# Optimization experiments

Measured on AMD Instinct MI355X. Metric: run time of the kernel, lower is better.

## Reference

```python
import jax, jax.numpy as jnp
import numpy as np

B, L, D, H = 8, 1024, 1024, 16
DH = D // H  # dim_per_head = 64
HG = H // 2  # global/local head split


def setup_inputs() -> dict:
    key = jax.random.key(0)
    ks = jax.random.split(key, 10)
    s = 1.0 / np.sqrt(D)
    return {
        "key": jax.random.normal(ks[0], (B, L, D), jnp.float32),
        "value": jax.random.normal(ks[1], (B, L, D), jnp.float32),
        "query": jax.random.normal(ks[2], (B, L, D), jnp.float32),
        "mask": jax.random.bernoulli(ks[3], 0.1, (B, L, L)),
        "additional_mask": jax.random.bernoulli(ks[4], 0.1, (B, L)),
        "Wk": jax.random.normal(ks[5], (D, D), jnp.float32) * s,
        "bk": jnp.zeros((D,), jnp.float32),
        "Wv": jax.random.normal(ks[6], (D, D), jnp.float32) * s,
        "bv": jnp.zeros((D,), jnp.float32),
        "Wq": jax.random.normal(ks[7], (D, D), jnp.float32) * s,
        "bq": jnp.zeros((D,), jnp.float32),
        "Wo": jax.random.normal(ks[8], (D, D), jnp.float32) * s,
        "bo": jnp.zeros((D,), jnp.float32),
    }


def _shape(x):
    # [B, L, D] -> [B, H, L, DH]
    return x.reshape(B, -1, H, DH).transpose(0, 2, 1, 3)


def reference(key, value, query, mask, additional_mask,
              Wk, bk, Wv, bv, Wq, bq, Wo, bo):
    # projections (torch Linear: x @ W.T + b)
    k = _shape(key @ Wk.T + bk)
    v = _shape(value @ Wv.T + bv)
    q = _shape(query @ Wq.T + bq) * (1.0 / np.sqrt(DH))  # scale query (edge_feature=None, additional_mask given)

    qg, ql = q[:, :HG], q[:, HG:]
    kg, kl = k[:, :HG], k[:, HG:]
    vg, vl = v[:, :HG], v[:, HG:]

    # global heads: standard masked attention
    score_g = jnp.einsum('bhqd,bhkd->bhqk', qg, kg)
    top_score = score_g[:, 0]  # taken BEFORE masking, as in original
    score_g = jnp.where(mask[:, None, :, :], -1e18, score_g)
    attn_g = jax.nn.softmax(score_g, axis=-1)  # dropout = identity (eval)
    ctx_g = jnp.einsum('bhqk,bhkd->bhqd', attn_g, vg)

    # local heads: additional_mask [B, k] broadcast over heads and queries
    score_l = jnp.einsum('bhqd,bhkd->bhqk', ql, kl)
    score_l = jnp.where(additional_mask[:, None, None, :], -1e18, score_l)
    attn_l = jax.nn.softmax(score_l, axis=-1)
    ctx_l = jnp.einsum('bhqk,bhkd->bhqd', attn_l, vl)

    ctx = jnp.concatenate([ctx_g, ctx_l], axis=1)          # [B, H, L, DH]
    ctx = ctx.transpose(0, 2, 1, 3).reshape(B, -1, D)      # unshape -> [B, L, D]
    out = ctx @ Wo.T + bo
    return out, top_score
```

## Files before the change

kernel.cpp:

```cpp
#include <hip/hip_runtime.h>
#include <hip/hip_bf16.h>

typedef unsigned short u16;
typedef unsigned int u32;
typedef __attribute__((ext_vector_type(8))) short short8;
typedef __attribute__((ext_vector_type(4))) short short4v;
typedef __attribute__((ext_vector_type(4))) float floatx4;

#define BB 8
#define LL 1024
#define DD 1024
#define HH 16
#define DHH 64
#define NEGBIG (-3.0e38f)
#define QSCALE 0.1803368801111204f
#define LN2F   0.6931471805599453f

__device__ inline u16 f2b(float f) {
  union { __hip_bfloat16 h; u16 u; } cv;
  cv.h = __float2bfloat16(f);
  return cv.u;
}
__device__ inline float b2f(u16 u) {
  union { u16 u; __hip_bfloat16 h; } cv;
  cv.u = u;
  return __bfloat162float(cv.h);
}
__device__ inline float fin(float v, float sentinel) {
  return (fabsf(v) < 1e30f) ? v : sentinel;
}
__device__ inline float fexp2(float x) {
#if __has_builtin(__builtin_amdgcn_exp2f)
  return __builtin_amdgcn_exp2f(x);
#else
  return exp2f(x);
#endif
}
__device__ inline void async16(const void* g, void* l) {
  __builtin_amdgcn_global_load_lds(
      (__attribute__((address_space(1))) void*)(const_cast<void*>(g)),
      (__attribute__((address_space(3))) void*)l, 16, 0, 0);
}


__global__ __launch_bounds__(256) void convpack(
    const float* __restrict__ key, const float* __restrict__ value,
    const float* __restrict__ Wk, const float* __restrict__ Wv,
    const float* __restrict__ Wq, const float* __restrict__ Wo,
    const int* __restrict__ mask, const int* __restrict__ amask,
    u16* __restrict__ keyb, u16* __restrict__ valb, u16* __restrict__ Wkb,
    u16* __restrict__ Wvb, u16* __restrict__ Wqb, u16* __restrict__ Wob,
    u32* __restrict__ maskb, u32* __restrict__ amaskb) {
  const int job = blockIdx.y;
  const int gtid = blockIdx.x * 256 + threadIdx.x;
  const int stride = gridDim.x * 256;

  if (job < 6) {
    const float* src; u16* dst; size_t n4;
    switch (job) {
      case 0: src = key;   dst = keyb; n4 = (size_t)BB * LL * DD / 4; break;
      case 1: src = value; dst = valb; n4 = (size_t)BB * LL * DD / 4; break;
      case 2: src = Wk;    dst = Wkb;  n4 = (size_t)DD * DD / 4; break;
      case 3: src = Wv;    dst = Wvb;  n4 = (size_t)DD * DD / 4; break;
      case 4: src = Wq;    dst = Wqb;  n4 = (size_t)DD * DD / 4; break;
      default: src = Wo;   dst = Wob;  n4 = (size_t)DD * DD / 4; break;
    }
    for (size_t i = gtid; i < n4; i += stride) {
      float4 v = ((const float4*)src)[i];
      short4v s;
      s[0] = (short)f2b(v.x); s[1] = (short)f2b(v.y);
      s[2] = (short)f2b(v.z); s[3] = (short)f2b(v.w);
      *(short4v*)(dst + i * 4) = s;
    }
  } else if (job == 6) {
    const size_t nw = (size_t)BB * LL * LL / 32;
    for (size_t w = gtid; w < nw; w += stride) {
      const int4* src = (const int4*)(mask + w * 32);
      u32 bits = 0;
#pragma unroll
      for (int c = 0; c < 8; c++) {
        int4 v = src[c];
        bits |= (u32)(v.x != 0) << (c * 4);
        bits |= (u32)(v.y != 0) << (c * 4 + 1);
        bits |= (u32)(v.z != 0) << (c * 4 + 2);
        bits |= (u32)(v.w != 0) << (c * 4 + 3);
      }
      maskb[w] = bits;
    }
  } else {
    const int nw = BB * LL / 32;
    for (int w = gtid; w < nw; w += stride) {
      const int4* src = (const int4*)(amask + w * 32);
      u32 bits = 0;
#pragma unroll
      for (int c = 0; c < 8; c++) {
        int4 v = src[c];
        bits |= (u32)(v.x != 0) << (c * 4);
        bits |= (u32)(v.y != 0) << (c * 4 + 1);
        bits |= (u32)(v.z != 0) << (c * 4 + 2);
        bits |= (u32)(v.w != 0) << (c * 4 + 3);
      }
      amaskb[w] = bits;
    }
  }
}

__global__ __launch_bounds__(256) void gemm_qkv(
    const u16* __restrict__ keyb, const u16* __restrict__ valb,
    const float* __restrict__ query, const u16* __restrict__ Wkb,
    const u16* __restrict__ Wvb, const u16* __restrict__ Wqb,
    const float* __restrict__ bk, const float* __restrict__ bv,
    const float* __restrict__ bq, u16* __restrict__ kbuf,
    u16* __restrict__ vbt, u16* __restrict__ qbuf) {
  __shared__ u16 As[128 * 32];
  __shared__ u16 Ws[128 * 32];

  const int z = blockIdx.z;
  const int tid = threadIdx.x;
  const int wave = tid >> 6, lane = tid & 63;
  const int lr = lane & 15, lq = lane >> 4;
  const int row0 = blockIdx.x * 128;
  const int col0 = blockIdx.y * 128;
  const int wm = (wave & 1) * 64, wn = (wave >> 1) * 64;

  floatx4 acc[4][4];
#pragma unroll
  for (int i = 0; i < 4; i++)
#pragma unroll
    for (int j = 0; j < 4; j++) acc[i][j] = (floatx4){0.f, 0.f, 0.f, 0.f};

  const int cc0 = tid, cc1 = 256 + tid;
  u16* As0 = As + wave * 512;
  u16* As1 = As + 2048 + wave * 512;
  u16* Ws0 = Ws + wave * 512;
  u16* Ws1 = Ws + 2048 + wave * 512;

  if (z < 2) {
    const u16* A  = (z == 0) ? keyb : valb;
    const u16* Wb = (z == 0) ? Wkb : Wvb;
    const u16* Ag0 = A + (size_t)(row0 + (cc0 >> 2)) * 1024 + (cc0 & 3) * 8;
    const u16* Ag1 = A + (size_t)(row0 + (cc1 >> 2)) * 1024 + (cc1 & 3) * 8;
    const u16* Wg0 = Wb + (size_t)(col0 + (cc0 >> 2)) * 1024 + (cc0 & 3) * 8;
    const u16* Wg1 = Wb + (size_t)(col0 + (cc1 >> 2)) * 1024 + (cc1 & 3) * 8;

    for (int k0 = 0; k0 < 1024; k0 += 32) {
      __syncthreads();
      async16(Ag0 + k0, As0);
      async16(Ag1 + k0, As1);
      async16(Wg0 + k0, Ws0);
      async16(Wg1 + k0, Ws1);
      __syncthreads();

      short8 af[4], wf[4];
#pragma unroll
      for (int mi = 0; mi < 4; mi++)
        af[mi] = *(const short8*)(As + (wm + mi * 16 + lr) * 32 + lq * 8);
#pragma unroll
      for (int ni = 0; ni < 4; ni++)
        wf[ni] = *(const short8*)(Ws + (wn + ni * 16 + lr) * 32 + lq * 8);
#pragma unroll
      for (int mi = 0; mi < 4; mi++)
#pragma unroll
        for (int ni = 0; ni < 4; ni++)
          acc[mi][ni] = __builtin_amdgcn_mfma_f32_16x16x32_bf16(af[mi], wf[ni],
                                                                acc[mi][ni], 0, 0, 0);
    }
  } else {
    const u16* Wg0 = Wqb + (size_t)(col0 + (cc0 >> 2)) * 1024 + (cc0 & 3) * 8;
    const u16* Wg1 = Wqb + (size_t)(col0 + (cc1 >> 2)) * 1024 + (cc1 & 3) * 8;

    for (int k0 = 0; k0 < 1024; k0 += 32) {
      float4 ag[4];
#pragma unroll
      for (int it = 0; it < 4; it++) {
        const int cc = it * 256 + tid;
        ag[it] = *(const float4*)(query + (size_t)(row0 + (cc >> 3)) * 1024 +
                                  (cc & 7) * 4 + k0);
      }
      __syncthreads();
      async16(Wg0 + k0, Ws0);
      async16(Wg1 + k0, Ws1);
#pragma unroll
      for (int it = 0; it < 4; it++) {
        const int cc = it * 256 + tid;
        short4v s;
        s[0] = (short)f2b(ag[it].x); s[1] = (short)f2b(ag[it].y);
        s[2] = (short)f2b(ag[it].z); s[3] = (short)f2b(ag[it].w);
        *(short4v*)(As + (cc >> 3) * 32 + (cc & 7) * 4) = s;
      }
      __syncthreads();

      short8 af[4], wf[4];
#pragma unroll
      for (int mi = 0; mi < 4; mi++)
        af[mi] = *(const short8*)(As + (wm + mi * 16 + lr) * 32 + lq * 8);
#pragma unroll
      for (int ni = 0; ni < 4; ni++)
        wf[ni] = *(const short8*)(Ws + (wn + ni * 16 + lr) * 32 + lq * 8);
#pragma unroll
      for (int mi = 0; mi < 4; mi++)
#pragma unroll
        for (int ni = 0; ni < 4; ni++)
          acc[mi][ni] = __builtin_amdgcn_mfma_f32_16x16x32_bf16(af[mi], wf[ni],
                                                                acc[mi][ni], 0, 0, 0);
    }
  }

  const float scale = (z == 2) ? QSCALE : 1.0f;
  const float* bias = (z == 0) ? bk : (z == 1) ? bv : bq;
  u16* outb = (z == 0) ? kbuf : qbuf;

#pragma unroll
  for (int ni = 0; ni < 4; ni++) {
    const int col = col0 + wn + ni * 16 + lr;
    const float bvv = bias[col];
#pragma unroll
    for (int mi = 0; mi < 4; mi++) {
#pragma unroll
      for (int r = 0; r < 4; r++) {
        const int row = row0 + wm + mi * 16 + lq * 4 + r;
        const float v = (acc[mi][ni][r] + bvv) * scale;
        const int b = row >> 10, l = row & 1023, h = col >> 6, dh = col & 63;
        if (z == 1)
          vbt[((b * HH + h) * DHH + dh) * LL + l] = f2b(v);
        else
          outb[((b * HH + h) * LL + l) * DHH + dh] = f2b(v);
      }
    }
  }
}

template <int OUT>
__global__ __launch_bounds__(256) void gemm_b(
    const u16* __restrict__ A, const u16* __restrict__ Wb,
    const float* __restrict__ bias, void* __restrict__ outv, float scale) {
  __shared__ u16 As[128 * 32];
  __shared__ u16 Ws[128 * 32];

  const int tid = threadIdx.x;
  const int wave = tid >> 6, lane = tid & 63;
  const int lr = lane & 15, lq = lane >> 4;
  const int row0 = blockIdx.x * 128;
  const int col0 = blockIdx.y * 128;
  const int wm = (wave & 1) * 64, wn = (wave >> 1) * 64;

  floatx4 acc[4][4];
#pragma unroll
  for (int i = 0; i < 4; i++)
#pragma unroll
    for (int j = 0; j < 4; j++) acc[i][j] = (floatx4){0.f, 0.f, 0.f, 0.f};

  const int cc0 = tid, cc1 = 256 + tid;
  const u16* Ag0 = A + (size_t)(row0 + (cc0 >> 2)) * 1024 + (cc0 & 3) * 8;
  const u16* Ag1 = A + (size_t)(row0 + (cc1 >> 2)) * 1024 + (cc1 & 3) * 8;
  const u16* Wg0 = Wb + (size_t)(col0 + (cc0 >> 2)) * 1024 + (cc0 & 3) * 8;
  const u16* Wg1 = Wb + (size_t)(col0 + (cc1 >> 2)) * 1024 + (cc1 & 3) * 8;
  u16* As0 = As + wave * 512;
  u16* As1 = As + 2048 + wave * 512;
  u16* Ws0 = Ws + wave * 512;
  u16* Ws1 = Ws + 2048 + wave * 512;

  for (int k0 = 0; k0 < 1024; k0 += 32) {
    __syncthreads();
    async16(Ag0 + k0, As0);
    async16(Ag1 + k0, As1);
    async16(Wg0 + k0, Ws0);
    async16(Wg1 + k0, Ws1);
    __syncthreads();

    short8 af[4], wf[4];
#pragma unroll
    for (int mi = 0; mi < 4; mi++)
      af[mi] = *(const short8*)(As + (wm + mi * 16 + lr) * 32 + lq * 8);
#pragma unroll
    for (int ni = 0; ni < 4; ni++)
      wf[ni] = *(const short8*)(Ws + (wn + ni * 16 + lr) * 32 + lq * 8);
#pragma unroll
    for (int mi = 0; mi < 4; mi++)
#pragma unroll
      for (int ni = 0; ni < 4; ni++)
        acc[mi][ni] = __builtin_amdgcn_mfma_f32_16x16x32_bf16(af[mi], wf[ni],
                                                              acc[mi][ni], 0, 0, 0);
  }

#pragma unroll
  for (int ni = 0; ni < 4; ni++) {
    const int col = col0 + wn + ni * 16 + lr;
    const float bv = bias[col];
#pragma unroll
    for (int mi = 0; mi < 4; mi++) {
#pragma unroll
      for (int r = 0; r < 4; r++) {
        const int row = row0 + wm + mi * 16 + lq * 4 + r;
        const float v = (acc[mi][ni][r] + bv) * scale;
        if (OUT == 0) {
          const int b = row >> 10, l = row & 1023, h = col >> 6, dh = col & 63;
          ((u16*)outv)[((b * HH + h) * LL + l) * DHH + dh] = f2b(v);
        } else if (OUT == 2) {
          const int b = row >> 10, l = row & 1023, h = col >> 6, dh = col & 63;
          ((u16*)outv)[((b * HH + h) * DHH + dh) * LL + l] = f2b(v);
        } else {
          ((float*)outv)[(size_t)row * 1024 + col] = v;
        }
      }
    }
  }
}

__global__ __launch_bounds__(256) void attn_fast(
    const u16* __restrict__ qbuf, const u16* __restrict__ kbuf,
    const u16* __restrict__ vbt, const u32* __restrict__ maskb,
    const u32* __restrict__ amaskb, u16* __restrict__ ctx,
    float* __restrict__ top) {
  __shared__ u16 Ks[2][64 * 64];
  __shared__ u16 Vts[2][64 * 64];

  const int id = blockIdx.x;
  const int xcd = id & 7;
  const int r_ = id >> 3;
  const int b = r_ & 7;
  const int h = (((r_ >> 3) & 1) << 3) | (xcd ^ b);
  const int qt = r_ >> 4;

  const int tid = threadIdx.x, wave = tid >> 6, lane = tid & 63;
  const int lr = lane & 15, lq = lane >> 4;
  const int lq4 = lq * 4;
  const int x7 = lr & 7;

  const u16* Qg = qbuf + (size_t)((b * HH + h) * LL + qt * 128) * DHH;
  const u16* Kg = kbuf + (size_t)((b * HH + h) * LL) * DHH;
  const u16* Vtg = vbt + (size_t)((b * HH + h) * DHH) * LL;

  short8 qf[2][2];
#pragma unroll
  for (int mi = 0; mi < 2; mi++)
#pragma unroll
    for (int kk = 0; kk < 2; kk++)
      qf[mi][kk] = *(const short8*)(Qg + (wave * 32 + mi * 16 + lr) * 64 +
                                    kk * 32 + lq * 8);

  const int g0 = tid, g1 = 256 + tid;
  const int kr0 = g0 >> 3, kc0 = (g0 & 7) ^ (kr0 & 7);
  const int kr1 = g1 >> 3, kc1 = (g1 & 7) ^ (kr1 & 7);
  const int cs0 = ((0 + lq) ^ x7) * 8;
  const int cs1 = ((4 + lq) ^ x7) * 8;
  const int lqh = lq >> 1, lqb = (lq & 1) * 4;
  const int go00 = ((0 + lqh) ^ x7) * 8 + lqb;
  const int go01 = ((2 + lqh) ^ x7) * 8 + lqb;
  const int go10 = ((4 + lqh) ^ x7) * 8 + lqb;
  const int go11 = ((6 + lqh) ^ x7) * 8 + lqb;

  auto stage = [&](int kc, int buf) {
    async16(Kg + kc * 4096 + kr0 * 64 + kc0 * 8, &Ks[buf][wave * 512]);
    async16(Kg + kc * 4096 + kr1 * 64 + kc1 * 8, &Ks[buf][2048 + wave * 512]);
    async16(Vtg + (size_t)kr0 * LL + kc * 64 + kc0 * 8, &Vts[buf][wave * 512]);
    async16(Vtg + (size_t)kr1 * LL + kc * 64 + kc1 * 8,
            &Vts[buf][2048 + wave * 512]);
  };

  float mrow[2], lrow[2];
  floatx4 Oacc[2][4];
#pragma unroll
  for (int mi = 0; mi < 2; mi++) {
    mrow[mi] = NEGBIG;
    lrow[mi] = 0.f;
#pragma unroll
    for (int ni = 0; ni < 4; ni++) Oacc[mi][ni] = (floatx4){0.f, 0.f, 0.f, 0.f};
  }

  stage(0, 0);

  for (int kc = 0; kc < 16; kc++) {
    const int cur = kc & 1;
    __syncthreads();
    if (kc < 15) stage(kc + 1, cur ^ 1);
    const u16* Ksc = Ks[cur];
    const u16* Vtsc = Vts[cur];

    floatx4 S[2][4];
    __builtin_amdgcn_s_setprio(1);
#pragma unroll
    for (int nj = 0; nj < 4; nj++) {
      const short8 kf0 = *(const short8*)(Ksc + (nj * 16 + lr) * 64 + cs0);
      const short8 kf1 = *(const short8*)(Ksc + (nj * 16 + lr) * 64 + cs1);
#pragma unroll
      for (int mi = 0; mi < 2; mi++) {
        floatx4 z = (floatx4){0.f, 0.f, 0.f, 0.f};
        z = __builtin_amdgcn_mfma_f32_16x16x32_bf16(kf1, qf[mi][1], z, 0, 0, 0);
        z = __builtin_amdgcn_mfma_f32_16x16x32_bf16(kf0, qf[mi][0], z, 0, 0, 0);
        S[mi][nj] = z;
      }
    }
    __builtin_amdgcn_s_setprio(0);

    short8 pf[2][2];
#pragma unroll
    for (int mi = 0; mi < 2; mi++) {
      const int row = qt * 128 + wave * 32 + mi * 16 + lr;

      if (h == 0) {
        float* tp = top + (size_t)(b * LL + row) * LL + kc * 64 + lq4;
#pragma unroll
        for (int nj = 0; nj < 4; nj++) {
          float4 t;
          t.x = S[mi][nj][0] * LN2F; t.y = S[mi][nj][1] * LN2F;
          t.z = S[mi][nj][2] * LN2F; t.w = S[mi][nj][3] * LN2F;
          *(float4*)(tp + nj * 16) = t;
        }
      }

      if (h < 8) {
        const uint2 mw =
            *(const uint2*)(maskb + (size_t)(b * LL + row) * 32 + kc * 2);
#pragma unroll
        for (int nj = 0; nj < 4; nj++) {
          const u32 nib = (((nj & 2) ? mw.y : mw.x) >> ((nj & 1) * 16 + lq4)) & 15u;
#pragma unroll
          for (int r = 0; r < 4; r++)
            if ((nib >> r) & 1) S[mi][nj][r] = -1e18f;
        }
      } else {
        const uint2 aw = *(const uint2*)(amaskb + b * 32 + kc * 2);
#pragma unroll
        for (int nj = 0; nj < 4; nj++) {
          const u32 nib = (((nj & 2) ? aw.y : aw.x) >> ((nj & 1) * 16 + lq4)) & 15u;
#pragma unroll
          for (int r = 0; r < 4; r++)
            if ((nib >> r) & 1) S[mi][nj][r] = -1e18f;
        }
      }

      float cm = fmaxf(fmaxf(S[mi][0][0], S[mi][0][1]),
                       fmaxf(S[mi][0][2], S[mi][0][3]));
#pragma unroll
      for (int nj = 1; nj < 4; nj++)
        cm = fmaxf(cm, fmaxf(fmaxf(S[mi][nj][0], S[mi][nj][1]),
                             fmaxf(S[mi][nj][2], S[mi][nj][3])));
      cm = fmaxf(cm, __shfl_xor(cm, 16, 64));
      cm = fmaxf(cm, __shfl_xor(cm, 32, 64));
      const float mold = mrow[mi];
      const float mnew = fmaxf(mold, cm);
      const float alpha = fexp2(mold - mnew);
      mrow[mi] = mnew;
      float rs = 0.f;
#pragma unroll
      for (int nj = 0; nj < 4; nj++)
#pragma unroll
        for (int r = 0; r < 4; r++) {
          const float p = fexp2(S[mi][nj][r] - mnew);
          S[mi][nj][r] = p;
          rs += p;
        }
      rs += __shfl_xor(rs, 16, 64);
      rs += __shfl_xor(rs, 32, 64);
      lrow[mi] = lrow[mi] * alpha + rs;
#pragma unroll
      for (int ni = 0; ni < 4; ni++)
#pragma unroll
        for (int r = 0; r < 4; r++) Oacc[mi][ni][r] *= alpha;

#pragma unroll
      for (int kk = 0; kk < 2; kk++) {
        short8 p;
#pragma unroll
        for (int r = 0; r < 4; r++) {
          p[r] = (short)f2b(S[mi][2 * kk][r]);
          p[4 + r] = (short)f2b(S[mi][2 * kk + 1][r]);
        }
        pf[mi][kk] = p;
      }
    }

    __builtin_amdgcn_s_setprio(1);
#pragma unroll
    for (int ni = 0; ni < 4; ni++) {
      const int rb = (ni * 16 + lr) * 64;
      const short4v v00 = *(const short4v*)(Vtsc + rb + go00);
      const short4v v01 = *(const short4v*)(Vtsc + rb + go01);
      const short4v v10 = *(const short4v*)(Vtsc + rb + go10);
      const short4v v11 = *(const short4v*)(Vtsc + rb + go11);
      const short8 vf0 = __builtin_shufflevector(v00, v01, 0, 1, 2, 3, 4, 5, 6, 7);
      const short8 vf1 = __builtin_shufflevector(v10, v11, 0, 1, 2, 3, 4, 5, 6, 7);
#pragma unroll
      for (int mi = 0; mi < 2; mi++) {
        Oacc[mi][ni] =
            __builtin_amdgcn_mfma_f32_16x16x32_bf16(vf0, pf[mi][0], Oacc[mi][ni], 0, 0, 0);
        Oacc[mi][ni] =
            __builtin_amdgcn_mfma_f32_16x16x32_bf16(vf1, pf[mi][1], Oacc[mi][ni], 0, 0, 0);
      }
    }
    __builtin_amdgcn_s_setprio(0);
  }

#pragma unroll
  for (int mi = 0; mi < 2; mi++) {
    const float inv = 1.0f / lrow[mi];
    const int row = qt * 128 + wave * 32 + mi * 16 + lr;
    u16* cp = ctx + (size_t)(b * LL + row) * DD + h * DHH + lq4;
#pragma unroll
    for (int ni = 0; ni < 4; ni++) {
      short4v o;
      o[0] = (short)f2b(Oacc[mi][ni][0] * inv);
      o[1] = (short)f2b(Oacc[mi][ni][1] * inv);
      o[2] = (short)f2b(Oacc[mi][ni][2] * inv);
      o[3] = (short)f2b(Oacc[mi][ni][3] * inv);
      *(short4v*)(cp + ni * 16) = o;
    }
  }
}

template <int MODE>
__global__ __launch_bounds__(256) void gemm_k(
    const void* __restrict__ Av, const float* __restrict__ W,
    const float* __restrict__ biasp, void* __restrict__ outv, float scale) {
  __shared__ u16 As[128 * 32];
  __shared__ u16 Ws[128 * 32];
  const int tid = threadIdx.x;
  const int wave = tid >> 6, lane = tid & 63;
  const int lr = lane & 15, lq = lane >> 4;
  const int row0 = blockIdx.x * 128;
  const int col0 = blockIdx.y * 128;
  const int wm = (wave & 1) * 64, wn = (wave >> 1) * 64;
  floatx4 acc[4][4];
#pragma unroll
  for (int i = 0; i < 4; i++)
#pragma unroll
    for (int j = 0; j < 4; j++) acc[i][j] = (floatx4){0.f, 0.f, 0.f, 0.f};
  const float* Af = (const float*)Av;
  const u16* Ab = (const u16*)Av;
  for (int k0 = 0; k0 < 1024; k0 += 32) {
    float4 wg[4];
#pragma unroll
    for (int it = 0; it < 4; it++) {
      const int cc = it * 256 + tid;
      wg[it] = *(const float4*)(W + (size_t)(col0 + (cc >> 3)) * 1024 + (cc & 7) * 4 + k0);
    }
    float4 ag[4];
    short8 ab0, ab1;
    if (MODE == 0) {
#pragma unroll
      for (int it = 0; it < 4; it++) {
        const int cc = it * 256 + tid;
        ag[it] = *(const float4*)(Af + (size_t)(row0 + (cc >> 3)) * 1024 + (cc & 7) * 4 + k0);
      }
    } else {
      const int cc0 = tid, cc1 = 256 + tid;
      ab0 = *(const short8*)(Ab + (size_t)(row0 + (cc0 >> 2)) * 1024 + (cc0 & 3) * 8 + k0);
      ab1 = *(const short8*)(Ab + (size_t)(row0 + (cc1 >> 2)) * 1024 + (cc1 & 3) * 8 + k0);
    }
    __syncthreads();
#pragma unroll
    for (int it = 0; it < 4; it++) {
      const int cc = it * 256 + tid;
      short4v s;
      s[0] = (short)f2b(wg[it].x); s[1] = (short)f2b(wg[it].y);
      s[2] = (short)f2b(wg[it].z); s[3] = (short)f2b(wg[it].w);
      *(short4v*)(Ws + (cc >> 3) * 32 + (cc & 7) * 4) = s;
    }
    if (MODE == 0) {
#pragma unroll
      for (int it = 0; it < 4; it++) {
        const int cc = it * 256 + tid;
        short4v s;
        s[0] = (short)f2b(ag[it].x); s[1] = (short)f2b(ag[it].y);
        s[2] = (short)f2b(ag[it].z); s[3] = (short)f2b(ag[it].w);
        *(short4v*)(As + (cc >> 3) * 32 + (cc & 7) * 4) = s;
      }
    } else {
      *(short8*)(As + tid * 8) = ab0;
      *(short8*)(As + (256 + tid) * 8) = ab1;
    }
    __syncthreads();
    short8 af[4], wf[4];
#pragma unroll
    for (int mi = 0; mi < 4; mi++)
      af[mi] = *(const short8*)(As + (wm + mi * 16 + lr) * 32 + lq * 8);
#pragma unroll
    for (int ni = 0; ni < 4; ni++)
      wf[ni] = *(const short8*)(Ws + (wn + ni * 16 + lr) * 32 + lq * 8);
#pragma unroll
    for (int mi = 0; mi < 4; mi++)
#pragma unroll
      for (int ni = 0; ni < 4; ni++)
        acc[mi][ni] = __builtin_amdgcn_mfma_f32_16x16x32_bf16(af[mi], wf[ni], acc[mi][ni], 0, 0, 0);
  }
#pragma unroll
  for (int ni = 0; ni < 4; ni++) {
    const int col = col0 + wn + ni * 16 + lr;
    const float bv = biasp[col];
#pragma unroll
    for (int mi = 0; mi < 4; mi++) {
#pragma unroll
      for (int r = 0; r < 4; r++) {
        const int row = row0 + wm + mi * 16 + lq * 4 + r;
        float v = (acc[mi][ni][r] + bv) * scale;
        v = fin(v, MODE == 0 ? 700.0f : 1000.0f);
        if (MODE == 0) {
          const int b = row >> 10, l = row & 1023, h = col >> 6, dh = col & 63;
          ((u16*)outv)[((b * HH + h) * LL + l) * DHH + dh] = f2b(v);
        } else {
          ((float*)outv)[(size_t)row * 1024 + col] = v;
        }
      }
    }
  }
}

__global__ __launch_bounds__(256) void attn_kernel(
    const u16* __restrict__ qbuf, const u16* __restrict__ kbuf,
    const u16* __restrict__ vbuf, const int* __restrict__ mask,
    const int* __restrict__ amask, u16* __restrict__ ctx,
    float* __restrict__ top) {
  __shared__ u16 Qs[128 * 64];
  __shared__ u16 Ks[64 * 64];
  __shared__ u16 Vts[64 * 64];
  __shared__ u16 Ps[4][32 * 64];
  const int qt = blockIdx.x, h = blockIdx.y, b = blockIdx.z;
  const int tid = threadIdx.x, wave = tid >> 6, lane = tid & 63;
  const int lr = lane & 15, lq = lane >> 4;
  const u16* Qg = qbuf + (size_t)((b * HH + h) * LL + qt * 128) * DHH;
  const u16* Kg = kbuf + (size_t)((b * HH + h) * LL) * DHH;
  const u16* Vg = vbuf + (size_t)((b * HH + h) * LL) * DHH;
#pragma unroll
  for (int it = 0; it < 4; it++) {
    short8 qv = *(const short8*)(Qg + (it * 256 + tid) * 8);
    *(short8*)(Qs + (it * 256 + tid) * 8) = qv;
  }
  float mrow[2][4], lrow[2][4];
  floatx4 Oacc[2][4];
#pragma unroll
  for (int mi = 0; mi < 2; mi++)
#pragma unroll
    for (int r = 0; r < 4; r++) { mrow[mi][r] = NEGBIG; lrow[mi][r] = 0.f; }
#pragma unroll
  for (int mi = 0; mi < 2; mi++)
#pragma unroll
    for (int ni = 0; ni < 4; ni++) Oacc[mi][ni] = (floatx4){0.f, 0.f, 0.f, 0.f};
  for (int kc = 0; kc < 16; kc++) {
    const u16* Kc = Kg + kc * 64 * DHH;
    const u16* Vc = Vg + kc * 64 * DHH;
    short8 kv0 = *(const short8*)(Kc + tid * 8);
    short8 kv1 = *(const short8*)(Kc + (256 + tid) * 8);
    short8 vv0 = *(const short8*)(Vc + tid * 8);
    short8 vv1 = *(const short8*)(Vc + (256 + tid) * 8);
    __syncthreads();
    *(short8*)(Ks + tid * 8) = kv0;
    *(short8*)(Ks + (256 + tid) * 8) = kv1;
    {
      const int r0 = tid >> 3, e0 = (tid & 7) * 8;
#pragma unroll
      for (int j = 0; j < 8; j++) Vts[(e0 + j) * 64 + r0] = (u16)vv0[j];
      const int cc1 = 256 + tid;
      const int r1 = cc1 >> 3, e1 = (cc1 & 7) * 8;
#pragma unroll
      for (int j = 0; j < 8; j++) Vts[(e1 + j) * 64 + r1] = (u16)vv1[j];
    }
    __syncthreads();
    floatx4 S[2][4];
    short8 qf[2][2];
#pragma unroll
    for (int mi = 0; mi < 2; mi++)
#pragma unroll
      for (int kk = 0; kk < 2; kk++)
        qf[mi][kk] = *(const short8*)(Qs + (wave * 32 + mi * 16 + lr) * 64 + kk * 32 + lq * 8);
#pragma unroll
    for (int nj = 0; nj < 4; nj++) {
      short8 kf0 = *(const short8*)(Ks + (nj * 16 + lr) * 64 + lq * 8);
      short8 kf1 = *(const short8*)(Ks + (nj * 16 + lr) * 64 + 32 + lq * 8);
#pragma unroll
      for (int mi = 0; mi < 2; mi++) {
        floatx4 z = (floatx4){0.f, 0.f, 0.f, 0.f};
        z = __builtin_amdgcn_mfma_f32_16x16x32_bf16(qf[mi][1], kf1, z, 0, 0, 0);
        z = __builtin_amdgcn_mfma_f32_16x16x32_bf16(qf[mi][0], kf0, z, 0, 0, 0);
        S[mi][nj] = z;
      }
    }
#pragma unroll
    for (int mi = 0; mi < 2; mi++)
#pragma unroll
      for (int nj = 0; nj < 4; nj++)
#pragma unroll
        for (int r = 0; r < 4; r++) S[mi][nj][r] = fin(S[mi][nj][r], 800.0f);
    if (h == 0) {
#pragma unroll
      for (int mi = 0; mi < 2; mi++)
#pragma unroll
        for (int nj = 0; nj < 4; nj++)
#pragma unroll
          for (int r = 0; r < 4; r++) {
            const int row = qt * 128 + wave * 32 + mi * 16 + lq * 4 + r;
            const int colk = kc * 64 + nj * 16 + lr;
            top[(size_t)(b * LL + row) * LL + colk] = S[mi][nj][r];
          }
    }
    if (h < 8) {
#pragma unroll
      for (int mi = 0; mi < 2; mi++)
#pragma unroll
        for (int r = 0; r < 4; r++) {
          const int row = qt * 128 + wave * 32 + mi * 16 + lq * 4 + r;
          const int* mp = mask + (size_t)(b * LL + row) * LL + kc * 64;
#pragma unroll
          for (int nj = 0; nj < 4; nj++) {
            const int mv = mp[nj * 16 + lr];
            S[mi][nj][r] = mv ? -1e18f : S[mi][nj][r];
          }
        }
    } else {
#pragma unroll
      for (int nj = 0; nj < 4; nj++) {
        const int mv = amask[b * LL + kc * 64 + nj * 16 + lr];
        if (mv) {
#pragma unroll
          for (int mi = 0; mi < 2; mi++)
#pragma unroll
            for (int r = 0; r < 4; r++) S[mi][nj][r] = -1e18f;
        }
      }
    }
#pragma unroll
    for (int mi = 0; mi < 2; mi++) {
#pragma unroll
      for (int r = 0; r < 4; r++) {
        float cm = S[mi][0][r];
#pragma unroll
        for (int nj = 1; nj < 4; nj++) cm = fmaxf(cm, S[mi][nj][r]);
#pragma unroll
        for (int off = 1; off < 16; off <<= 1) cm = fmaxf(cm, __shfl_xor(cm, off, 64));
        const float mold = mrow[mi][r];
        const float mnew = fmaxf(mold, cm);
        const float alpha = __expf(mold - mnew);
        mrow[mi][r] = mnew;
        float rs = 0.f;
#pragma unroll
        for (int nj = 0; nj < 4; nj++) {
          const float p = __expf(S[mi][nj][r] - mnew);
          S[mi][nj][r] = p;
          rs += p;
        }
#pragma unroll
        for (int off = 1; off < 16; off <<= 1) rs += __shfl_xor(rs, off, 64);
        lrow[mi][r] = lrow[mi][r] * alpha + rs;
#pragma unroll
        for (int ni = 0; ni < 4; ni++) Oacc[mi][ni][r] *= alpha;
      }
    }
#pragma unroll
    for (int mi = 0; mi < 2; mi++)
#pragma unroll
      for (int nj = 0; nj < 4; nj++)
#pragma unroll
        for (int r = 0; r < 4; r++)
          Ps[wave][(mi * 16 + lq * 4 + r) * 64 + nj * 16 + lr] = f2b(S[mi][nj][r]);
    __syncthreads();
#pragma unroll
    for (int kk = 0; kk < 2; kk++) {
      short8 pf[2];
#pragma unroll
      for (int mi = 0; mi < 2; mi++)
        pf[mi] = *(const short8*)(&Ps[wave][(mi * 16 + lr) * 64 + kk * 32 + lq * 8]);
#pragma unroll
      for (int ni = 0; ni < 4; ni++) {
        short8 vf = *(const short8*)(Vts + (ni * 16 + lr) * 64 + kk * 32 + lq * 8);
#pragma unroll
        for (int mi = 0; mi < 2; mi++)
          Oacc[mi][ni] = __builtin_amdgcn_mfma_f32_16x16x32_bf16(pf[mi], vf, Oacc[mi][ni], 0, 0, 0);
      }
    }
  }
#pragma unroll
  for (int mi = 0; mi < 2; mi++)
#pragma unroll
    for (int r = 0; r < 4; r++) {
      const float inv = 1.0f / lrow[mi][r];
      const int row = qt * 128 + wave * 32 + mi * 16 + lq * 4 + r;
#pragma unroll
      for (int ni = 0; ni < 4; ni++) {
        const int col = h * DHH + ni * 16 + lr;
        ctx[(size_t)(b * LL + row) * DD + col] = f2b(fin(Oacc[mi][ni][r] * inv, 900.0f));
      }
    }
}

extern "C" void kernel_launch(void* const* d_in, const int* in_sizes, int n_in,
                              void* d_out, int out_size, void* d_ws, size_t ws_size,
                              hipStream_t stream) {
  const float* key   = (const float*)d_in[0];
  const float* value = (const float*)d_in[1];
  const float* query = (const float*)d_in[2];
  const int* mask    = (const int*)d_in[3];
  const int* amask   = (const int*)d_in[4];
  const float* Wk = (const float*)d_in[5];
  const float* bk = (const float*)d_in[6];
  const float* Wv = (const float*)d_in[7];
  const float* bv = (const float*)d_in[8];
  const float* Wq = (const float*)d_in[9];
  const float* bq = (const float*)d_in[10];
  const float* Wo = (const float*)d_in[11];
  const float* bo = (const float*)d_in[12];

  float* outp = (float*)d_out;
  float* topp = outp + (size_t)BB * LL * DD;

  const size_t M8 = (size_t)BB * LL * DD;
  const size_t M1 = (size_t)DD * DD;
  const size_t NEED = (size_t)90 * 1024 * 1024;

  dim3 tb(256), gg(64, 8, 1), ga(8, 16, 8);

  if (ws_size >= NEED) {
    u16* W16 = (u16*)d_ws;
    u16* keyb = W16;
    u16* valb = W16 + M8;
    u16* qbuf = W16 + 2 * M8;
    u16* Wkb = W16 + 3 * M8;
    u16* Wvb = Wkb + M1;
    u16* Wqb = Wvb + M1;
    u16* Wob = Wqb + M1;
    u32* maskb = (u32*)(Wob + M1);
    u32* amaskb = maskb + 262144;
    u16* kbuf = W16 + 3 * M8 + 5 * M1;
    u16* vbt  = kbuf + M8;
    u16* cbuf = valb;

    convpack<<<dim3(256, 8), tb, 0, stream>>>(
        key, value, Wk, Wv, Wq, Wo, mask, amask,
        keyb, valb, Wkb, Wvb, Wqb, Wob, maskb, amaskb);
    gemm_qkv<<<dim3(64, 8, 3), tb, 0, stream>>>(
        keyb, valb, query, Wkb, Wvb, Wqb, bk, bv, bq, kbuf, vbt, qbuf);
    attn_fast<<<dim3(1024, 1, 1), tb, 0, stream>>>(qbuf, kbuf, vbt, maskb,
                                                   amaskb, cbuf, topp);
    gemm_b<1><<<gg, tb, 0, stream>>>(cbuf, Wob, bo, outp, 1.0f);
  } else {
    u16* kbuf = (u16*)d_ws;
    u16* vbuf = kbuf + M8;
    u16* qbuf = vbuf + M8;
    u16* cbuf = qbuf + M8;
    gemm_k<0><<<gg, tb, 0, stream>>>(key,   Wk, bk, kbuf, 1.0f);
    gemm_k<0><<<gg, tb, 0, stream>>>(value, Wv, bv, vbuf, 1.0f);
    gemm_k<0><<<gg, tb, 0, stream>>>(query, Wq, bq, qbuf, 0.125f);
    attn_kernel<<<ga, tb, 0, stream>>>(qbuf, kbuf, vbuf, mask, amask, cbuf, topp);
    gemm_k<1><<<gg, tb, 0, stream>>>(cbuf, Wo, bo, outp, 1.0f);
  }
}
```

Before: 428.4 us.

## Fuse key/value bf16 conversion into QKV GEMM, double-buffer it, defer softmax rescale

The separate fp32-to-bf16 conversion of key and value is removed from convpack. gemm_qkv now loads fp32 activations for all three projections and converts them in registers, which avoids writing and re-reading two large bf16 intermediates. The GEMM main loop is double-buffered in LDS, so the next tile's W async load and A register load overlap the MFMAs, with one barrier per iteration. In attention, mask words are prefetched one chunk ahead and the global/local mask branches are unified. The online-softmax rescale is skipped unless the running max grows by more than a threshold, which trades exactness of the running max for fewer exp and multiply operations and relies on exp2 headroom to avoid overflow.

```diff
diff --git a/kernel.cpp b/kernel.cpp
--- a/kernel.cpp
+++ b/kernel.cpp
@@ -15,6 +15,7 @@
 #define NEGBIG (-3.0e38f)
 #define QSCALE 0.1803368801111204f
 #define LN2F   0.6931471805599453f
+#define DEFER_THR 12.0f
 
 __device__ inline u16 f2b(float f) {
   union { __hip_bfloat16 h; u16 u; } cv;
@@ -44,27 +45,24 @@
 
 
 __global__ __launch_bounds__(256) void convpack(
-    const float* __restrict__ key, const float* __restrict__ value,
     const float* __restrict__ Wk, const float* __restrict__ Wv,
     const float* __restrict__ Wq, const float* __restrict__ Wo,
     const int* __restrict__ mask, const int* __restrict__ amask,
-    u16* __restrict__ keyb, u16* __restrict__ valb, u16* __restrict__ Wkb,
-    u16* __restrict__ Wvb, u16* __restrict__ Wqb, u16* __restrict__ Wob,
-    u32* __restrict__ maskb, u32* __restrict__ amaskb) {
+    u16* __restrict__ Wkb, u16* __restrict__ Wvb, u16* __restrict__ Wqb,
+    u16* __restrict__ Wob, u32* __restrict__ maskb, u32* __restrict__ amaskb) {
   const int job = blockIdx.y;
   const int gtid = blockIdx.x * 256 + threadIdx.x;
   const int stride = gridDim.x * 256;
 
-  if (job < 6) {
-    const float* src; u16* dst; size_t n4;
+  if (job < 4) {
+    const float* src; u16* dst;
     switch (job) {
-      case 0: src = key;   dst = keyb; n4 = (size_t)BB * LL * DD / 4; break;
-      case 1: src = value; dst = valb; n4 = (size_t)BB * LL * DD / 4; break;
-      case 2: src = Wk;    dst = Wkb;  n4 = (size_t)DD * DD / 4; break;
-      case 3: src = Wv;    dst = Wvb;  n4 = (size_t)DD * DD / 4; break;
-      case 4: src = Wq;    dst = Wqb;  n4 = (size_t)DD * DD / 4; break;
-      default: src = Wo;   dst = Wob;  n4 = (size_t)DD * DD / 4; break;
-    }
+      case 0: src = Wk; dst = Wkb; break;
+      case 1: src = Wv; dst = Wvb; break;
+      case 2: src = Wq; dst = Wqb; break;
+      default: src = Wo; dst = Wob; break;
+    }
+    const size_t n4 = (size_t)DD * DD / 4;
     for (size_t i = gtid; i < n4; i += stride) {
       float4 v = ((const float4*)src)[i];
       short4v s;
@@ -72,7 +70,7 @@
       s[2] = (short)f2b(v.z); s[3] = (short)f2b(v.w);
       *(short4v*)(dst + i * 4) = s;
     }
-  } else if (job == 6) {
+  } else if (job == 4) {
     const size_t nw = (size_t)BB * LL * LL / 32;
     for (size_t w = gtid; w < nw; w += stride) {
       const int4* src = (const int4*)(mask + w * 32);
@@ -106,14 +104,14 @@
 }
 
 __global__ __launch_bounds__(256) void gemm_qkv(
-    const u16* __restrict__ keyb, const u16* __restrict__ valb,
+    const float* __restrict__ key, const float* __restrict__ value,
     const float* __restrict__ query, const u16* __restrict__ Wkb,
     const u16* __restrict__ Wvb, const u16* __restrict__ Wqb,
     const float* __restrict__ bk, const float* __restrict__ bv,
     const float* __restrict__ bq, u16* __restrict__ kbuf,
     u16* __restrict__ vbt, u16* __restrict__ qbuf) {
-  __shared__ u16 As[128 * 32];
-  __shared__ u16 Ws[128 * 32];
+  __shared__ u16 As[2][128 * 32];
+  __shared__ u16 Ws[2][128 * 32];
 
   const int z = blockIdx.z;
   const int tid = threadIdx.x;
@@ -129,81 +127,68 @@
 #pragma unroll
     for (int j = 0; j < 4; j++) acc[i][j] = (floatx4){0.f, 0.f, 0.f, 0.f};
 
+  const float* A = (z == 0) ? key : (z == 1) ? value : query;
+  const u16* Wb  = (z == 0) ? Wkb : (z == 1) ? Wvb : Wqb;
+
   const int cc0 = tid, cc1 = 256 + tid;
-  u16* As0 = As + wave * 512;
-  u16* As1 = As + 2048 + wave * 512;
-  u16* Ws0 = Ws + wave * 512;
-  u16* Ws1 = Ws + 2048 + wave * 512;
-
-  if (z < 2) {
-    const u16* A  = (z == 0) ? keyb : valb;
-    const u16* Wb = (z == 0) ? Wkb : Wvb;
-    const u16* Ag0 = A + (size_t)(row0 + (cc0 >> 2)) * 1024 + (cc0 & 3) * 8;
-    const u16* Ag1 = A + (size_t)(row0 + (cc1 >> 2)) * 1024 + (cc1 & 3) * 8;
-    const u16* Wg0 = Wb + (size_t)(col0 + (cc0 >> 2)) * 1024 + (cc0 & 3) * 8;
-    const u16* Wg1 = Wb + (size_t)(col0 + (cc1 >> 2)) * 1024 + (cc1 & 3) * 8;
-
-    for (int k0 = 0; k0 < 1024; k0 += 32) {
-      __syncthreads();
-      async16(Ag0 + k0, As0);
-      async16(Ag1 + k0, As1);
-      async16(Wg0 + k0, Ws0);
-      async16(Wg1 + k0, Ws1);
-      __syncthreads();
-
-      short8 af[4], wf[4];
-#pragma unroll
-      for (int mi = 0; mi < 4; mi++)
-        af[mi] = *(const short8*)(As + (wm + mi * 16 + lr) * 32 + lq * 8);
+  const u16* Wg0 = Wb + (size_t)(col0 + (cc0 >> 2)) * 1024 + (cc0 & 3) * 8;
+  const u16* Wg1 = Wb + (size_t)(col0 + (cc1 >> 2)) * 1024 + (cc1 & 3) * 8;
+
+  auto stageW = [&](int t, int buf) {
+    const int o = t * 32;
+    async16(Wg0 + o, &Ws[buf][wave * 512]);
+    async16(Wg1 + o, &Ws[buf][2048 + wave * 512]);
+  };
+  auto loadA = [&](int t, float4* ag) {
+#pragma unroll
+    for (int it = 0; it < 4; it++) {
+      const int cc = it * 256 + tid;
+      ag[it] = *(const float4*)(A + (size_t)(row0 + (cc >> 3)) * 1024 +
+                                (cc & 7) * 4 + t * 32);
+    }
+  };
+  auto writeA = [&](int buf, const float4* ag) {
+#pragma unroll
+    for (int it = 0; it < 4; it++) {
+      const int cc = it * 256 + tid;
+      short4v s;
+      s[0] = (short)f2b(ag[it].x); s[1] = (short)f2b(ag[it].y);
+      s[2] = (short)f2b(ag[it].z); s[3] = (short)f2b(ag[it].w);
+      *(short4v*)(&As[buf][(cc >> 3) * 32 + (cc & 7) * 4]) = s;
+    }
+  };
+
+  {
+    float4 ag0[4];
+    loadA(0, ag0);
+    stageW(0, 0);
+    writeA(0, ag0);
+  }
+
+  for (int t = 0; t < 32; t++) {
+    const int buf = t & 1;
+    __syncthreads();
+    float4 ag[4];
+    if (t < 31) {
+      stageW(t + 1, buf ^ 1);
+      loadA(t + 1, ag);
+    }
+
+    short8 af[4], wf[4];
+#pragma unroll
+    for (int mi = 0; mi < 4; mi++)
+      af[mi] = *(const short8*)(&As[buf][(wm + mi * 16 + lr) * 32 + lq * 8]);
+#pragma unroll
+    for (int ni = 0; ni < 4; ni++)
+      wf[ni] = *(const short8*)(&Ws[buf][(wn + ni * 16 + lr) * 32 + lq * 8]);
+#pragma unroll
+    for (int mi = 0; mi < 4; mi++)
 #pragma unroll
       for (int ni = 0; ni < 4; ni++)
-        wf[ni] = *(const short8*)(Ws + (wn + ni * 16 + lr) * 32 + lq * 8);
-#pragma unroll
-      for (int mi = 0; mi < 4; mi++)
-#pragma unroll
-        for (int ni = 0; ni < 4; ni++)
-          acc[mi][ni] = __builtin_amdgcn_mfma_f32_16x16x32_bf16(af[mi], wf[ni],
-                                                                acc[mi][ni], 0, 0, 0);
-    }
-  } else {
-    const u16* Wg0 = Wqb + (size_t)(col0 + (cc0 >> 2)) * 1024 + (cc0 & 3) * 8;
-    const u16* Wg1 = Wqb + (size_t)(col0 + (cc1 >> 2)) * 1024 + (cc1 & 3) * 8;
-
-    for (int k0 = 0; k0 < 1024; k0 += 32) {
-      float4 ag[4];
-#pragma unroll
-      for (int it = 0; it < 4; it++) {
-        const int cc = it * 256 + tid;
-        ag[it] = *(const float4*)(query + (size_t)(row0 + (cc >> 3)) * 1024 +
-                                  (cc & 7) * 4 + k0);
-      }
-      __syncthreads();
-      async16(Wg0 + k0, Ws0);
-      async16(Wg1 + k0, Ws1);
-#pragma unroll
-      for (int it = 0; it < 4; it++) {
-        const int cc = it * 256 + tid;
-        short4v s;
-        s[0] = (short)f2b(ag[it].x); s[1] = (short)f2b(ag[it].y);
-        s[2] = (short)f2b(ag[it].z); s[3] = (short)f2b(ag[it].w);
-        *(short4v*)(As + (cc >> 3) * 32 + (cc & 7) * 4) = s;
-      }
-      __syncthreads();
-
-      short8 af[4], wf[4];
-#pragma unroll
-      for (int mi = 0; mi < 4; mi++)
-        af[mi] = *(const short8*)(As + (wm + mi * 16 + lr) * 32 + lq * 8);
-#pragma unroll
-      for (int ni = 0; ni < 4; ni++)
-        wf[ni] = *(const short8*)(Ws + (wn + ni * 16 + lr) * 32 + lq * 8);
-#pragma unroll
-      for (int mi = 0; mi < 4; mi++)
-#pragma unroll
-        for (int ni = 0; ni < 4; ni++)
-          acc[mi][ni] = __builtin_amdgcn_mfma_f32_16x16x32_bf16(af[mi], wf[ni],
-                                                                acc[mi][ni], 0, 0, 0);
-    }
+        acc[mi][ni] = __builtin_amdgcn_mfma_f32_16x16x32_bf16(af[mi], wf[ni],
+                                                              acc[mi][ni], 0, 0, 0);
+
+    if (t < 31) writeA(buf ^ 1, ag);
   }
 
   const float scale = (z == 2) ? QSCALE : 1.0f;
@@ -358,6 +343,15 @@
             &Vts[buf][2048 + wave * 512]);
   };
 
+  const int rowm0 = qt * 128 + wave * 32 + lr;
+  const int rowm1 = rowm0 + 16;
+  const u32* mb0 = (h < 8) ? maskb + (size_t)(b * LL + rowm0) * 32
+                           : amaskb + b * 32;
+  const u32* mb1 = (h < 8) ? maskb + (size_t)(b * LL + rowm1) * 32
+                           : amaskb + b * 32;
+  uint2 mwc0 = *(const uint2*)(mb0);
+  uint2 mwc1 = *(const uint2*)(mb1);
+
   float mrow[2], lrow[2];
   floatx4 Oacc[2][4];
 #pragma unroll
@@ -373,7 +367,12 @@
   for (int kc = 0; kc < 16; kc++) {
     const int cur = kc & 1;
     __syncthreads();
-    if (kc < 15) stage(kc + 1, cur ^ 1);
+    uint2 mwn0, mwn1;
+    if (kc < 15) {
+      stage(kc + 1, cur ^ 1);
+      mwn0 = *(const uint2*)(mb0 + (kc + 1) * 2);
+      mwn1 = *(const uint2*)(mb1 + (kc + 1) * 2);
+    }
     const u16* Ksc = Ks[cur];
     const u16* Vtsc = Vts[cur];
 
@@ -409,21 +408,11 @@
         }
       }
 
-      if (h < 8) {
-        const uint2 mw =
-            *(const uint2*)(maskb + (size_t)(b * LL + row) * 32 + kc * 2);
+      {
+        const uint2 mw = mi ? mwc1 : mwc0;
 #pragma unroll
         for (int nj = 0; nj < 4; nj++) {
           const u32 nib = (((nj & 2) ? mw.y : mw.x) >> ((nj & 1) * 16 + lq4)) & 15u;
-#pragma unroll
-          for (int r = 0; r < 4; r++)
-            if ((nib >> r) & 1) S[mi][nj][r] = -1e18f;
-        }
-      } else {
-        const uint2 aw = *(const uint2*)(amaskb + b * 32 + kc * 2);
-#pragma unroll
-        for (int nj = 0; nj < 4; nj++) {
-          const u32 nib = (((nj & 2) ? aw.y : aw.x) >> ((nj & 1) * 16 + lq4)) & 15u;
 #pragma unroll
           for (int r = 0; r < 4; r++)
             if ((nib >> r) & 1) S[mi][nj][r] = -1e18f;
@@ -439,25 +428,29 @@
       cm = fmaxf(cm, __shfl_xor(cm, 16, 64));
       cm = fmaxf(cm, __shfl_xor(cm, 32, 64));
       const float mold = mrow[mi];
-      const float mnew = fmaxf(mold, cm);
-      const float alpha = fexp2(mold - mnew);
-      mrow[mi] = mnew;
+      if (!__all(cm <= mold + DEFER_THR)) {
+        const float mnew = fmaxf(mold, cm);
+        const float alpha = fexp2(mold - mnew);
+        mrow[mi] = mnew;
+        lrow[mi] *= alpha;
+#pragma unroll
+        for (int ni = 0; ni < 4; ni++)
+#pragma unroll
+          for (int r = 0; r < 4; r++) Oacc[mi][ni][r] *= alpha;
+      }
+      const float mcur = mrow[mi];
       float rs = 0.f;
 #pragma unroll
       for (int nj = 0; nj < 4; nj++)
 #pragma unroll
         for (int r = 0; r < 4; r++) {
-          const float p = fexp2(S[mi][nj][r] - mnew);
+          const float p = fexp2(S[mi][nj][r] - mcur);
           S[mi][nj][r] = p;
           rs += p;
         }
       rs += __shfl_xor(rs, 16, 64);
       rs += __shfl_xor(rs, 32, 64);
-      lrow[mi] = lrow[mi] * alpha + rs;
-#pragma unroll
-      for (int ni = 0; ni < 4; ni++)
-#pragma unroll
-        for (int r = 0; r < 4; r++) Oacc[mi][ni][r] *= alpha;
+      lrow[mi] += rs;
 
 #pragma unroll
       for (int kk = 0; kk < 2; kk++) {
@@ -490,6 +483,8 @@
       }
     }
     __builtin_amdgcn_s_setprio(0);
+
+    if (kc < 15) { mwc0 = mwn0; mwc1 = mwn1; }
   }
 
 #pragma unroll
@@ -810,24 +805,21 @@
 
   if (ws_size >= NEED) {
     u16* W16 = (u16*)d_ws;
-    u16* keyb = W16;
-    u16* valb = W16 + M8;
-    u16* qbuf = W16 + 2 * M8;
-    u16* Wkb = W16 + 3 * M8;
+    u16* Wkb = W16;
     u16* Wvb = Wkb + M1;
     u16* Wqb = Wvb + M1;
     u16* Wob = Wqb + M1;
     u32* maskb = (u32*)(Wob + M1);
     u32* amaskb = maskb + 262144;
-    u16* kbuf = W16 + 3 * M8 + 5 * M1;
+    u16* kbuf = W16 + 6 * M1;
     u16* vbt  = kbuf + M8;
-    u16* cbuf = valb;
-
-    convpack<<<dim3(256, 8), tb, 0, stream>>>(
-        key, value, Wk, Wv, Wq, Wo, mask, amask,
-        keyb, valb, Wkb, Wvb, Wqb, Wob, maskb, amaskb);
+    u16* qbuf = vbt + M8;
+    u16* cbuf = qbuf + M8;
+
+    convpack<<<dim3(256, 6), tb, 0, stream>>>(
+        Wk, Wv, Wq, Wo, mask, amask, Wkb, Wvb, Wqb, Wob, maskb, amaskb);
     gemm_qkv<<<dim3(64, 8, 3), tb, 0, stream>>>(
-        keyb, valb, query, Wkb, Wvb, Wqb, bk, bv, bq, kbuf, vbt, qbuf);
+        key, value, query, Wkb, Wvb, Wqb, bk, bv, bq, kbuf, vbt, qbuf);
     attn_fast<<<dim3(1024, 1, 1), tb, 0, stream>>>(qbuf, kbuf, vbt, maskb,
                                                    amaskb, cbuf, topp);
     gemm_b<1><<<gg, tb, 0, stream>>>(cbuf, Wob, bo, outp, 1.0f);
```

Result: faster. 412.9 us (-3.6%).
